# Kernel optimization log

Hardware: AMD Instinct MI355X
Metric: run time of the kernel (lower is better)

Reference implementation:

```python
import jax, jax.numpy as jnp
import numpy as np

B, N, M, K = 2, 16384, 16384, 32
C_IN, C_OUT, KS = 64, 128, 15
RADIUS = 0.1
SIGMA = 0.5 * RADIUS  # module sets self.sigma = sigma * radius


def _generate_kernel_points(num_kpoints: int, radius: float) -> np.ndarray:
    # Fibonacci-sphere placement, matching the torch generate_kernel_points
    if num_kpoints == 1:
        return np.zeros((1, 3), dtype=np.float32)
    pts = np.zeros((num_kpoints, 3), dtype=np.float32)
    golden_angle = np.pi * (3 - np.sqrt(5))
    for i in range(num_kpoints):
        y = 1 - i / float(num_kpoints - 1) * 2
        r_y = np.sqrt(1 - y * y)
        theta = golden_angle * i
        pts[i] = np.array([np.cos(theta) * r_y, y, np.sin(theta) * r_y]) * radius
    return pts


def setup_inputs() -> dict:
    key = jax.random.key(0)
    k1, k2, k3, k4 = jax.random.split(key, 4)
    query_points = jax.random.uniform(k1, (B, N, 3), dtype=jnp.float32)
    support_points = jax.random.uniform(k2, (B, M, 3), dtype=jnp.float32)
    support_features = jax.random.normal(k3, (B, M, C_IN), dtype=jnp.float32)
    neighbor_idx = jax.random.randint(k4, (B, N, K), 0, M)
    kernel_points = jnp.asarray(_generate_kernel_points(KS, RADIUS * 0.8))
    k5 = jax.random.fold_in(key, 5)
    # kaiming-uniform-ish init on flattened (KS*C_IN, C_OUT)
    bound = np.sqrt(1.0 / (KS * C_IN))
    weights = jax.random.uniform(k5, (KS, C_IN, C_OUT), dtype=jnp.float32,
                                 minval=-bound, maxval=bound)
    bias = jnp.zeros((C_OUT,), dtype=jnp.float32)
    return {
        "query_points": query_points,
        "support_points": support_points,
        "support_features": support_features,
        "neighbor_idx": neighbor_idx,
        "kernel_points": kernel_points,
        "weights": weights,
        "bias": bias,
    }


def reference(query_points, support_points, support_features, neighbor_idx,
              kernel_points, weights, bias):
    # Batched gather: support[b, idx[b]] -> [B, N, K, *]
    gather = jax.vmap(lambda feats, idx: feats[idx])
    neighbor_points = gather(support_points, neighbor_idx)      # [B,N,K,3]
    neighbor_features = gather(support_features, neighbor_idx)  # [B,N,K,C_in]

    rel = neighbor_points - query_points[:, :, None, :]          # [B,N,K,3]
    # squared distance to each kernel point: [B,N,K,J]
    sq_dist = jnp.sum((rel[:, :, :, None, :] - kernel_points[None, None, None]) ** 2,
                      axis=-1)
    influences = jnp.exp(-sq_dist / (2 * SIGMA ** 2))
    influences = influences / (influences.sum(axis=-1, keepdims=True) + 1e-6)

    out = jnp.einsum('bnkc,bnkj,jco->bno', neighbor_features, influences, weights)
    return out + bias
```

## Files before the change

### kernel.cpp

```cpp
#include <hip/hip_runtime.h>
#include <hip/hip_bf16.h>


#define NB   16384
#define MB   16384
#define KN   32
#define CIN  64
#define COUT 128
#define KS   15
#define TP   32
#define PROW 2064
#define WF_BYTES  245760u
#define FP_BYTES  (2u * MB * CIN * 2u)
#define SP4_BYTES (2u * MB * 16u)

typedef __attribute__((ext_vector_type(8))) short short8;
typedef __attribute__((ext_vector_type(4))) float f32x4;

#define ROR_ADD(s, ctrl) \
    ((s) + __int_as_float(__builtin_amdgcn_update_dpp( \
        0, __float_as_int(s), (ctrl), 0xF, 0xF, true)))

static __device__ __forceinline__ unsigned int pack2_bf16(float f0, float f1) {
    const unsigned int a = __float_as_uint(f0) + 0x8000u;
    const unsigned int b = __float_as_uint(f1) + 0x8000u;
    return (a >> 16) | (b & 0xffff0000u);
}

static __device__ __forceinline__ unsigned int pack2_bf16_rne(float f0, float f1) {
    unsigned int a = __float_as_uint(f0);
    unsigned int b = __float_as_uint(f1);
    a += 0x7fffu + ((a >> 16) & 1u);
    b += 0x7fffu + ((b >> 16) & 1u);
    return (a >> 16) | (b & 0xffff0000u);
}

static __device__ __forceinline__ unsigned short f32_to_bf16_rne(float x) {
    unsigned int u = __float_as_uint(x);
    u += 0x7fffu + ((u >> 16) & 1u);
    return (unsigned short)(u >> 16);
}

__global__ __launch_bounds__(256)
void prep_kernel(const float* __restrict__ Wg, const float* __restrict__ feats,
                 const float* __restrict__ sp,
                 unsigned short* __restrict__ wf, unsigned int* __restrict__ fp,
                 float4* __restrict__ sp4, int full) {
    const int bid = blockIdx.x;
    if (bid < 60) {
        const int tid = bid * 256 + threadIdx.x;
        const int l = tid & 63;
        const int t = (tid >> 6) & 7;
        const int s = tid >> 9;
        const int n  = t * 16 + (l & 15);
        const int kb = s * 32 + (l >> 4) * 8;
        short8 o;
        #pragma unroll
        for (int i = 0; i < 8; ++i)
            o[i] = (short)f32_to_bf16_rne(Wg[(kb + i) * COUT + n]);
        *(short8*)(wf + (size_t)tid * 8) = o;
    } else if (!full) {
        return;
    } else if (bid < 60 + 128) {
        const int m = (bid - 60) * 256 + threadIdx.x;
        const float* s3 = sp + 3 * (size_t)m;
        sp4[m] = make_float4(s3[0], s3[1], s3[2], 0.0f);
    } else {
        const unsigned int t = (unsigned int)(bid - 188) * 256u + threadIdx.x;
        if (t < 2u * MB * 32u) {
            const int m   = t >> 5;
            const int p2  = t & 31;
            const int n16 = p2 >> 1;
            const int tt  = (p2 & 1) * 2;
            const float a = feats[(size_t)m * CIN + tt * 16 + n16];
            const float b = feats[(size_t)m * CIN + (tt + 1) * 16 + n16];
            fp[t] = pack2_bf16_rne(a, b);
        }
    }
}

template<bool PK>
__global__ __launch_bounds__(512, 4)
void kpconv_mfma(const float* __restrict__ qp,
                 const float* __restrict__ sp,
                 const float* __restrict__ feats,
                 const unsigned int* __restrict__ fpk,
                 const float4* __restrict__ sp4,
                 const int* __restrict__ nidx,
                 const float* __restrict__ kp,
                 const unsigned short* __restrict__ wfrag,
                 const float* __restrict__ bias,
                 float* __restrict__ out) {
    __shared__ __align__(16) char sF[TP * PROW];

    const int tid  = threadIdx.x;
    const int lane = tid & 63;
    const int wv   = tid >> 6;
    const int gp_base = blockIdx.x * TP;
    const int b = gp_base >> 14;
    const float*        fbf  = feats + (size_t)b * MB * CIN;
    const unsigned int* fpb  = fpk + (size_t)b * MB * 32;
    const float4*       sp4b = sp4 + (size_t)b * MB;
    const float*        spb  = sp + (size_t)b * MB * 3;

    const int n16  = lane & 15;
    const int quad = lane >> 4;

    float kxj, kyj, kzj;
    if (n16 < 15) {
        kxj = kp[3 * n16 + 0];
        kyj = kp[3 * n16 + 1];
        kzj = kp[3 * n16 + 2];
    } else {
        kxj = 1.0e4f; kyj = 1.0e4f; kzj = 1.0e4f;
    }

    const int gp0 = gp_base + wv * 4;
    const int* ip = nidx + (size_t)gp0 * KN + quad * 8;
    int4 nx0 = *(const int4*)(ip);
    int4 nx1 = *(const int4*)(ip + 4);

    #pragma unroll 1
    for (int pt = 0; pt < 4; ++pt) {
        const int pl = wv * 4 + pt;
        const int gp = gp0 + pt;

        int idxv[8];
        *(int4*)(&idxv[0]) = nx0;
        *(int4*)(&idxv[4]) = nx1;
        if (pt < 3) {
            const int* ipn = ip + (pt + 1) * KN;
            nx0 = *(const int4*)(ipn);
            nx1 = *(const int4*)(ipn + 4);
        }

        const float qx = qp[3 * gp + 0];
        const float qy = qp[3 * gp + 1];
        const float qz = qp[3 * gp + 2];
        const float qkx = qx + kxj, qky = qy + kyj, qkz = qz + kzj;

        float e[8];
        uint2 g[8];
        if (PK) {
            float4 s4[8];
            #pragma unroll
            for (int i = 0; i < 8; ++i) s4[i] = sp4b[idxv[i]];
            #pragma unroll
            for (int i = 0; i < 8; ++i)
                g[i] = *(const uint2*)(fpb + (size_t)idxv[i] * 32 + n16 * 2);
            #pragma unroll
            for (int i = 0; i < 8; ++i) {
                const float dx = s4[i].x - qkx;
                const float dy = s4[i].y - qky;
                const float dz = s4[i].z - qkz;
                const float d2 = fmaf(dx, dx, fmaf(dy, dy, dz * dz));
                e[i] = __expf(-200.0f * d2);
            }
        } else {
            #pragma unroll
            for (int i = 0; i < 8; ++i) {
                const float* s3 = spb + (size_t)idxv[i] * 3;
                const float dx = s3[0] - qkx;
                const float dy = s3[1] - qky;
                const float dz = s3[2] - qkz;
                const float d2 = fmaf(dx, dx, fmaf(dy, dy, dz * dz));
                e[i] = __expf(-200.0f * d2);
            }
        }

        unsigned int iu[4];
        float en[8];
        #pragma unroll
        for (int i = 0; i < 8; ++i) {
            float s = e[i];
            s = ROR_ADD(s, 0x128);
            s = ROR_ADD(s, 0x124);
            s = ROR_ADD(s, 0x122);
            s = ROR_ADD(s, 0x121);
            en[i] = e[i] * __builtin_amdgcn_rcpf(s + 1e-6f);
        }
        #pragma unroll
        for (int ih = 0; ih < 4; ++ih)
            iu[ih] = pack2_bf16(en[2 * ih], en[2 * ih + 1]);
        const short8 ifrag = *(const short8*)iu;

        unsigned int fu[4][4];
        if (PK) {
            #pragma unroll
            for (int ih = 0; ih < 4; ++ih) {
                const unsigned int ax = g[2 * ih].x, bx = g[2 * ih + 1].x;
                const unsigned int ay = g[2 * ih].y, by = g[2 * ih + 1].y;
                fu[0][ih] = __builtin_amdgcn_perm(bx, ax, 0x05040100u);
                fu[1][ih] = __builtin_amdgcn_perm(bx, ax, 0x07060302u);
                fu[2][ih] = __builtin_amdgcn_perm(by, ay, 0x05040100u);
                fu[3][ih] = __builtin_amdgcn_perm(by, ay, 0x07060302u);
            }
        } else {
            #pragma unroll
            for (int ih = 0; ih < 4; ++ih) {
                const float* fr0 = fbf + (size_t)idxv[2 * ih]     * CIN + n16;
                const float* fr1 = fbf + (size_t)idxv[2 * ih + 1] * CIN + n16;
                #pragma unroll
                for (int t = 0; t < 4; ++t)
                    fu[t][ih] = pack2_bf16(fr0[t * 16], fr1[t * 16]);
            }
        }

        #pragma unroll
        for (int t = 0; t < 4; ++t) {
            const short8 ffrag = *(const short8*)(fu[t]);
            f32x4 z = {0.f, 0.f, 0.f, 0.f};
            const f32x4 dd = __builtin_amdgcn_mfma_f32_16x16x32_bf16(ffrag, ifrag, z, 0, 0, 0);
            const unsigned int lo = pack2_bf16(dd[0], dd[1]);
            const unsigned int hi = pack2_bf16(dd[2], dd[3]);
            const int off = pl * PROW + n16 * 128 +
                            ((t * 32 + quad * 8) ^ ((n16 & 7) << 4));
            uint2 v; v.x = lo; v.y = hi;
            *(uint2*)(sF + off) = v;
        }
    }
    __syncthreads();

    const int mt = wv & 1;
    const int np = wv >> 1;
    const int t0 = np * 2, t1 = np * 2 + 1;
    f32x4 acc0 = {0.f, 0.f, 0.f, 0.f};
    f32x4 acc1 = {0.f, 0.f, 0.f, 0.f};
    const char* aBase = sF + (size_t)(mt * 16 + n16) * PROW;

    #pragma unroll
    for (int s = 0; s < 30; ++s) {
        const int j   = s >> 1;
        const int c0b = (s & 1) * 64 + quad * 16;
        const int off = j * 128 + (c0b ^ ((j & 7) << 4));
        const short8 a  = *(const short8*)(aBase + off);
        const short8 b0 = *(const short8*)(wfrag + ((size_t)(s * 8 + t0) * 64 + lane) * 8);
        const short8 b1 = *(const short8*)(wfrag + ((size_t)(s * 8 + t1) * 64 + lane) * 8);
        acc0 = __builtin_amdgcn_mfma_f32_16x16x32_bf16(a, b0, acc0, 0, 0, 0);
        acc1 = __builtin_amdgcn_mfma_f32_16x16x32_bf16(a, b1, acc1, 0, 0, 0);
    }

    const float bs0 = bias[t0 * 16 + n16];
    const float bs1 = bias[t1 * 16 + n16];
    #pragma unroll
    for (int r = 0; r < 4; ++r) {
        const int pr = mt * 16 + quad * 4 + r;
        out[(size_t)(gp_base + pr) * COUT + t0 * 16 + n16] = acc0[r] + bs0;
        out[(size_t)(gp_base + pr) * COUT + t1 * 16 + n16] = acc1[r] + bs1;
    }
}

extern "C" void kernel_launch(void* const* d_in, const int* in_sizes, int n_in,
                              void* d_out, int out_size, void* d_ws, size_t ws_size,
                              hipStream_t stream) {
    const float* qp = (const float*)d_in[0];
    const float* sp = (const float*)d_in[1];
    const float* ft = (const float*)d_in[2];
    const int*   ni = (const int*)d_in[3];
    const float* kp = (const float*)d_in[4];
    const float* wg = (const float*)d_in[5];
    const float* bs = (const float*)d_in[6];
    float* o = (float*)d_out;

    unsigned short* wfrag = (unsigned short*)d_ws;
    unsigned int*   fpk   = (unsigned int*)((char*)d_ws + WF_BYTES);
    float4*         sp4   = (float4*)((char*)d_ws + WF_BYTES + FP_BYTES);
    const int full = (ws_size >= (size_t)(WF_BYTES + FP_BYTES + SP4_BYTES)) ? 1 : 0;

    const int prep_blocks = full ? (60 + 128 + 4096) : 60;
    hipLaunchKernelGGL(prep_kernel, dim3(prep_blocks), dim3(256), 0, stream,
                       wg, ft, sp, wfrag, fpk, sp4, full);

    if (full) {
        hipLaunchKernelGGL((kpconv_mfma<true>), dim3((2 * NB) / TP), dim3(512), 0, stream,
                           qp, sp, ft, fpk, sp4, ni, kp, wfrag, bs, o);
    } else {
        hipLaunchKernelGGL((kpconv_mfma<false>), dim3((2 * NB) / TP), dim3(512), 0, stream,
                           qp, sp, ft, fpk, sp4, ni, kp, wfrag, bs, o);
    }
}
```

Baseline: 115.7 us.

## Halve per-block point tile to 16 and re-layout shared influence buffer

Each block now handles 16 query points instead of 32. Each of 8 waves computes 2 points in the first phase and one 16-column output tile in the second. The shared buffer is reorganised with a new XOR swizzle, and occupancy hints rise from 4 to 6 blocks per CU. The aim is more resident blocks and less LDS per block to hide gather latency. The cost is that each wave loads twice as much weight data per output, since a weight fragment is reused over 16 points instead of 32.

```diff
diff --git a/kernel.cpp b/kernel.cpp
--- a/kernel.cpp
+++ b/kernel.cpp
@@ -8,8 +8,7 @@
 #define CIN  64
 #define COUT 128
 #define KS   15
-#define TP   32
-#define PROW 2064
+#define TP   16
 #define WF_BYTES  245760u
 #define FP_BYTES  (2u * MB * CIN * 2u)
 #define SP4_BYTES (2u * MB * 16u)
@@ -80,7 +79,7 @@
 }
 
 template<bool PK>
-__global__ __launch_bounds__(512, 4)
+__global__ __launch_bounds__(512, 6)
 void kpconv_mfma(const float* __restrict__ qp,
                  const float* __restrict__ sp,
                  const float* __restrict__ feats,
@@ -91,7 +90,7 @@
                  const unsigned short* __restrict__ wfrag,
                  const float* __restrict__ bias,
                  float* __restrict__ out) {
-    __shared__ __align__(16) char sF[TP * PROW];
+    __shared__ __align__(16) char sF[16 * 2048];
 
     const int tid  = threadIdx.x;
     const int lane = tid & 63;
@@ -115,24 +114,20 @@
         kxj = 1.0e4f; kyj = 1.0e4f; kzj = 1.0e4f;
     }
 
-    const int gp0 = gp_base + wv * 4;
+    const int gp0 = gp_base + wv * 2;
     const int* ip = nidx + (size_t)gp0 * KN + quad * 8;
-    int4 nx0 = *(const int4*)(ip);
-    int4 nx1 = *(const int4*)(ip + 4);
-
-    #pragma unroll 1
-    for (int pt = 0; pt < 4; ++pt) {
-        const int pl = wv * 4 + pt;
+
+    int idx0[8], idx1[8];
+    *(int4*)(&idx0[0]) = *(const int4*)(ip);
+    *(int4*)(&idx0[4]) = *(const int4*)(ip + 4);
+    *(int4*)(&idx1[0]) = *(const int4*)(ip + KN);
+    *(int4*)(&idx1[4]) = *(const int4*)(ip + KN + 4);
+
+    #pragma unroll
+    for (int pt = 0; pt < 2; ++pt) {
+        const int pl = wv * 2 + pt;
         const int gp = gp0 + pt;
-
-        int idxv[8];
-        *(int4*)(&idxv[0]) = nx0;
-        *(int4*)(&idxv[4]) = nx1;
-        if (pt < 3) {
-            const int* ipn = ip + (pt + 1) * KN;
-            nx0 = *(const int4*)(ipn);
-            nx1 = *(const int4*)(ipn + 4);
-        }
+        const int* idxv = pt ? idx1 : idx0;
 
         const float qx = qp[3 * gp + 0];
         const float qy = qp[3 * gp + 1];
@@ -213,40 +208,30 @@
             const f32x4 dd = __builtin_amdgcn_mfma_f32_16x16x32_bf16(ffrag, ifrag, z, 0, 0, 0);
             const unsigned int lo = pack2_bf16(dd[0], dd[1]);
             const unsigned int hi = pack2_bf16(dd[2], dd[3]);
-            const int off = pl * PROW + n16 * 128 +
-                            ((t * 32 + quad * 8) ^ ((n16 & 7) << 4));
+            const int off = n16 * 2048 + (t * 2 + (quad >> 1)) * 256 +
+                            ((pl ^ (n16 & 7)) * 16) + (quad & 1) * 8;
             uint2 v; v.x = lo; v.y = hi;
             *(uint2*)(sF + off) = v;
         }
     }
     __syncthreads();
 
-    const int mt = wv & 1;
-    const int np = wv >> 1;
-    const int t0 = np * 2, t1 = np * 2 + 1;
-    f32x4 acc0 = {0.f, 0.f, 0.f, 0.f};
-    f32x4 acc1 = {0.f, 0.f, 0.f, 0.f};
-    const char* aBase = sF + (size_t)(mt * 16 + n16) * PROW;
+    f32x4 acc = {0.f, 0.f, 0.f, 0.f};
 
     #pragma unroll
     for (int s = 0; s < 30; ++s) {
-        const int j   = s >> 1;
-        const int c0b = (s & 1) * 64 + quad * 16;
-        const int off = j * 128 + (c0b ^ ((j & 7) << 4));
-        const short8 a  = *(const short8*)(aBase + off);
-        const short8 b0 = *(const short8*)(wfrag + ((size_t)(s * 8 + t0) * 64 + lane) * 8);
-        const short8 b1 = *(const short8*)(wfrag + ((size_t)(s * 8 + t1) * 64 + lane) * 8);
-        acc0 = __builtin_amdgcn_mfma_f32_16x16x32_bf16(a, b0, acc0, 0, 0, 0);
-        acc1 = __builtin_amdgcn_mfma_f32_16x16x32_bf16(a, b1, acc1, 0, 0, 0);
-    }
-
-    const float bs0 = bias[t0 * 16 + n16];
-    const float bs1 = bias[t1 * 16 + n16];
+        const int j = s >> 1;
+        const int u = (s & 1) * 4 + quad;
+        const int off = j * 2048 + u * 256 + ((n16 ^ (j & 7)) * 16);
+        const short8 a  = *(const short8*)(sF + off);
+        const short8 bf = *(const short8*)(wfrag + ((size_t)(s * 8 + wv) * 64 + lane) * 8);
+        acc = __builtin_amdgcn_mfma_f32_16x16x32_bf16(a, bf, acc, 0, 0, 0);
+    }
+
+    const float bsv = bias[wv * 16 + n16];
     #pragma unroll
     for (int r = 0; r < 4; ++r) {
-        const int pr = mt * 16 + quad * 4 + r;
-        out[(size_t)(gp_base + pr) * COUT + t0 * 16 + n16] = acc0[r] + bs0;
-        out[(size_t)(gp_base + pr) * COUT + t1 * 16 + n16] = acc1[r] + bs1;
+        out[(size_t)(gp_base + quad * 4 + r) * COUT + wv * 16 + n16] = acc[r] + bsv;
     }
 }
 
```

After: 115.7 us. Within noise of the previous version (+0.0%).
